# Kernel optimization log

Measured on AMD Instinct MI355X. Metric: run time of the kernel, lower is better.

Reference implementation:

```python
import jax, jax.numpy as jnp
import numpy as np

N, C_IN, T, V = 64, 64, 64, 25
C_OUT = 64
DK = DV = 16
NH = 8
DKH, DVH = DK // NH, DV // NH
KT = 9
EPS = 1e-5


def make_pe(channel, joint_num, time_len):
    # temporal positional encoding: position index = frame id, repeated per joint
    pos = np.repeat(np.arange(time_len), joint_num).astype(np.float32)[:, None]
    pe = np.zeros((time_len * joint_num, channel), np.float32)
    div = np.exp(np.arange(0, channel, 2).astype(np.float32) * -(np.log(10000.0) / channel))
    pe[:, 0::2] = np.sin(pos * div)
    pe[:, 1::2] = np.cos(pos * div)
    return jnp.asarray(pe.reshape(time_len, joint_num, channel).transpose(2, 0, 1)[None])  # (1,C,time,joint)


def setup_inputs():
    key = jax.random.key(0)
    ks = jax.random.split(key, 17)
    rn = lambda k, s, sc=0.05: jax.random.normal(k, s, jnp.float32) * sc
    return {
        'x': jax.random.normal(ks[0], (N, C_IN, T, V), jnp.float32),
        'pe': make_pe(C_IN, V, 64),
        'data_bn_g': 1.0 + rn(ks[1], (C_IN * V,)),
        'data_bn_b': rn(ks[2], (C_IN * V,)),
        'qkv_w': rn(ks[3], (3 * DK + DV, C_IN), 0.1),
        'qkv_b': rn(ks[4], (3 * DK + DV,)),
        'attn_w': rn(ks[5], (DV, DV), 0.1),
        'attn_b': rn(ks[6], (DV,)),
        'tcn_w': rn(ks[7], (C_OUT - DV, C_IN, KT, 1), 0.05),
        'tcn_b': rn(ks[8], (C_OUT - DV,)),
        'tcn_bn_g': 1.0 + rn(ks[9], (C_OUT - DV,)),
        'tcn_bn_b': rn(ks[10], (C_OUT - DV,)),
        'fc1_w': rn(ks[11], (C_OUT // 2, C_OUT), 0.1),
        'fc1_b': rn(ks[12], (C_OUT // 2,)),
        'fc2_w': rn(ks[13], (C_OUT, C_OUT // 2), 0.1),
        'fc2_b': rn(ks[14], (C_OUT,)),
        'bn_g': 1.0 + rn(ks[15], (C_OUT,)),
        'bn_b': rn(ks[16], (C_OUT,)),
    }


def _bn_eval(x, g, b, axis=1):
    # eval-mode BatchNorm with running_mean=0, running_var=1
    shape = [1] * x.ndim
    shape[axis] = -1
    scale = g / jnp.sqrt(1.0 + EPS)
    return x * scale.reshape(shape) + b.reshape(shape)


def _qkv_heads(x2d, qkv_w, qkv_b):
    # x2d: (B, C, T); 1x1 conv == channel matmul; split q/k/g/v, g is projected but unused
    qkv = jnp.einsum('oc,bct->bot', qkv_w, x2d) + qkv_b[None, :, None]
    q, k, _g, v = jnp.split(qkv, [DK, 2 * DK, 3 * DK], axis=1)
    B = x2d.shape[0]
    split = lambda z, ch: z.reshape(B, NH, ch // NH, -1)  # (B, Nh, chh, T)
    q = split(q, DK) * (DKH ** -0.5)
    return q, split(k, DK), split(v, DV)


def reference(x, pe, data_bn_g, data_bn_b, qkv_w, qkv_b, attn_w, attn_b,
              tcn_w, tcn_b, tcn_bn_g, tcn_bn_b, fc1_w, fc1_b, fc2_w, fc2_b, bn_g, bn_b):
    y = x + pe[:, :, :T]                                 # positional encoding (N,C,T,V)
    x_sum = x
    # data_bn over flattened (C*V) channels
    xb = x.transpose(0, 1, 3, 2).reshape(N, C_IN * V, T)
    xb = _bn_eval(xb, data_bn_g, data_bn_b)
    xn = xb.reshape(N, C_IN, V, T).transpose(0, 1, 3, 2)  # (N,C,T,V)
    # fold joints into batch: (N*V, C, T)
    xf = xn.transpose(0, 3, 1, 2).reshape(N * V, C_IN, T)
    yf = y.transpose(0, 3, 1, 2).reshape(N * V, C_IN, T)
    fq, fk, fv = _qkv_heads(xf, qkv_w, qkv_b)
    pq, pk, _ = _qkv_heads(yf, qkv_w, qkv_b)
    mu_q = fq.mean(-1, keepdims=True)                     # (B,H,dkh,1)
    fqc = fq - mu_q
    logits_pos = jnp.einsum('bhcs,bhct->bhst', pq, pk)    # (B,H,T,T)
    pairwise = jnp.einsum('bhcs,bhct->bhst', fqc, fk)     # (B,H,T,T)
    unary = jnp.einsum('bhcs,bhct->bhst', mu_q, fk)       # (B,H,1,T)
    weights = jnp.tanh(pairwise + logits_pos) + jnp.tanh(unary + logits_pos)
    ao = jnp.einsum('bhst,bhct->bhsc', weights, fv)       # (B,H,T,dvh)
    # (B,H,1,T,dvh) -> permute(0,1,4,2,3) -> combine heads -> (B, DV, T)
    ao = ao.transpose(0, 1, 3, 2).reshape(N * V, DV, T)
    ao = jnp.einsum('oc,bct->bot', attn_w, ao) + attn_b[None, :, None]
    ao = ao.reshape(N, V, DV, T).transpose(0, 2, 3, 1)    # (N, DV, T, V)
    # temporal conv branch (Unit2D: conv(k=9 temporal) + eval BN)
    tc = jax.lax.conv_general_dilated(x_sum, tcn_w, (1, 1), ((KT // 2, KT // 2), (0, 0)),
                                      dimension_numbers=('NCHW', 'OIHW', 'NCHW'))
    tc = tc + tcn_b[None, :, None, None]
    tc = _bn_eval(tc, tcn_bn_g, tcn_bn_b)
    result = jnp.concatenate([tc, ao], axis=1) + x_sum    # residual (down is None)
    # SE-style channel gating
    se = result.mean(axis=(2, 3))                         # (N, C_OUT)
    gate = jax.nn.sigmoid(jax.nn.relu(se @ fc1_w.T + fc1_b) @ fc2_w.T + fc2_b)
    result = result * gate[:, :, None, None] + result
    result = _bn_eval(result, bn_g, bn_b)
    return jax.nn.relu(result)
```

## Files before the change

### kernel.cpp

```cpp
#include <hip/hip_runtime.h>
#include <hip/hip_bf16.h>
#include <math.h>

#define TV_ 1600
#define SCALE_K 2.885390081777927f
#define RS2_ 0.70710678118654752f

typedef __attribute__((ext_vector_type(8))) short bf16x8;
typedef __attribute__((ext_vector_type(4))) float f32x4;
typedef __attribute__((ext_vector_type(2))) __fp16 h2f;

__device__ __forceinline__ float tanh_scaled(float y) {
    y = fminf(44.f, fmaxf(-44.f, y));
    float e = __builtin_amdgcn_exp2f(y);
    float r = __builtin_amdgcn_rcpf(e + 1.f);
    return __builtin_fmaf(e, r, -r);
}

__device__ __forceinline__ ushort f2bf(float f) {
    __hip_bfloat16 h = __float2bfloat16(f);
    return *(ushort*)&h;
}
__device__ __forceinline__ float bf2f(ushort u) {
    uint w = ((uint)u) << 16;
    return __uint_as_float(w);
}

__global__ __launch_bounds__(256) void prep_kernel(
    const float* __restrict__ tcn_w, const float* __restrict__ tg,
    const float* __restrict__ qkv_w, const float* __restrict__ qkv_b,
    const float* __restrict__ pe,
    ushort* __restrict__ wb, ushort* __restrict__ wq, float* __restrict__ qb,
    ushort* __restrict__ pet)
{
    int idx = blockIdx.x * 256 + threadIdx.x;
    if (idx < 27648) {
        int oc = idx / 576, kk = idx - oc * 576;
        int kt = kk >> 6, ci = kk & 63;
        float a = tg[oc] * rsqrtf(1.f + 1e-5f);
        wb[idx] = f2bf(tcn_w[(oc * 64 + ci) * 9 + kt] * a);
    } else if (idx < 32768) {
        int i2 = idx - 27648;
        int r = i2 >> 6, c = i2 & 63;
        int src; float sc;
        if (r < 16)      { src = r;      sc = RS2_; }
        else if (r < 32) { src = r;      sc = SCALE_K; }
        else if (r < 48) { src = r + 16; sc = 1.f; }
        else if (r < 64) { src = r - 48; sc = RS2_; }
        else             { src = r - 48; sc = SCALE_K; }
        wq[i2] = f2bf(qkv_w[src * 64 + c] * sc);
    } else if (idx < 32848) {
        int r = idx - 32768;
        int src; float sc;
        if (r < 16)      { src = r;      sc = RS2_; }
        else if (r < 32) { src = r;      sc = SCALE_K; }
        else if (r < 48) { src = r + 16; sc = 1.f; }
        else if (r < 64) { src = r - 48; sc = RS2_; }
        else             { src = r - 48; sc = SCALE_K; }
        qb[r] = qkv_b[src] * sc;
    } else if (idx < 32848 + 102400) {
        int i3 = idx - 32848;
        int ci = i3 / 1600, tv = i3 - ci * 1600;
        pet[tv * 64 + ci] = f2bf(pe[ci * 1600 + tv]);
    }
}

__global__ __launch_bounds__(256) void transpose_kernel(
    const float* __restrict__ x, ushort* __restrict__ rt, float* __restrict__ se)
{
    __shared__ ushort smt[64 * 66];
    const int tid = threadIdx.x;
    const int tv0 = blockIdx.x * 64;
    const int n = blockIdx.y;
    const int tvl = tid & 63, cig = tid >> 6;
    const int tv = tv0 + tvl;

    float psum[4] = {0.f, 0.f, 0.f, 0.f};
    #pragma unroll
    for (int k = 0; k < 16; ++k) {
        int ci = k * 4 + cig;
        float xv = x[(n * 64 + ci) * TV_ + tv];
        smt[tvl * 66 + ci] = f2bf(xv);
        if (k >= 12) psum[k - 12] += xv;
    }
    #pragma unroll
    for (int j = 0; j < 4; ++j) {
        float s = psum[j];
        #pragma unroll
        for (int off = 32; off >= 1; off >>= 1) s += __shfl_down(s, off, 64);
        if (tvl == 0) atomicAdd(&se[n * 64 + 48 + j * 4 + cig], s);
    }
    __syncthreads();

    #pragma unroll
    for (int j = 0; j < 8; ++j) {
        int chunk = tid + j * 256;
        int tvr = chunk >> 5, p = chunk & 31;
        uint val = *(const uint*)&smt[tvr * 66 + p * 2];
        *(uint*)&rt[(n * TV_ + tv0 + tvr) * 64 + p * 2] = val;
    }
}

__global__ __launch_bounds__(256, 5) void score_kernel(
    const ushort* __restrict__ rt, const ushort* __restrict__ pet,
    const float* __restrict__ dbg, const float* __restrict__ dbb,
    const ushort* __restrict__ wq, const float* __restrict__ qb,
    const float* __restrict__ attn_w, const float* __restrict__ attn_b,
    float* __restrict__ aoc, float* __restrict__ se)
{
    __shared__ float sm[5312];
    ushort* smu = (ushort*)sm;
    const int MU_ = 1056, AO = 1120;
    const int FKP = 2400, PKP = 2976, FVP = 3552, PQP = 4128, FQP = 4704;

    const int b = blockIdx.x;
    const int l = b >> 3;
    const int n = (b & 7) * 8 + l / 25;
    const int v = l % 25;
    const int tid = threadIdx.x;

    const int lane = tid & 63, wave = tid >> 6;
    const int m16 = lane & 15, q = lane >> 4;

    {
        const int part = tid & 7;
        const int ci0 = part * 8;
        const float rs = rsqrtf(1.f + 1e-5f);
        float sc8[8], sh8[8];
        #pragma unroll
        for (int i = 0; i < 8; ++i) {
            sc8[i] = dbg[(ci0 + i) * 25 + v] * rs;
            sh8[i] = dbb[(ci0 + i) * 25 + v];
        }
        #pragma unroll
        for (int j = 0; j < 2; ++j) {
            int t = (tid + j * 256) >> 3;
            uint4 xr = *(const uint4*)&rt[(n * TV_ + t * 25 + v) * 64 + ci0];
            uint4 pr = *(const uint4*)&pet[(t * 25 + v) * 64 + ci0];
            const ushort* xu = (const ushort*)&xr;
            const ushort* pu = (const ushort*)&pr;
            ushort xs[8], ys[8];
            #pragma unroll
            for (int i = 0; i < 8; ++i) {
                float xf = bf2f(xu[i]);
                xs[i] = f2bf(xf * sc8[i] + sh8[i]);
                ys[i] = f2bf(xf + bf2f(pu[i]));
            }
            *(uint4*)&smu[t * 72 + ci0] = *(uint4*)xs;
            *(uint4*)&smu[4608 + t * 72 + ci0] = *(uint4*)ys;
        }
    }
    __syncthreads();

    f32x4 acc[5];
    #pragma unroll
    for (int mt = 0; mt < 5; ++mt) acc[mt] = (f32x4){0.f, 0.f, 0.f, 0.f};
    #pragma unroll
    for (int kt = 0; kt < 2; ++kt) {
        const int koff = kt * 32 + q * 8;
        bf16x8 bx = *(const bf16x8*)&smu[(wave * 16 + m16) * 72 + koff];
        bf16x8 by = *(const bf16x8*)&smu[4608 + (wave * 16 + m16) * 72 + koff];
        #pragma unroll
        for (int mt = 0; mt < 5; ++mt) {
            bf16x8 a = *(const bf16x8*)&wq[(mt * 16 + m16) * 64 + koff];
            acc[mt] = __builtin_amdgcn_mfma_f32_16x16x32_bf16(a, (mt < 3) ? bx : by, acc[mt], 0, 0, 0);
        }
    }
    __syncthreads();

    {
        const int t = wave * 16 + m16;
        #pragma unroll
        for (int r = 0; r < 4; ++r)
            sm[(q * 4 + r) * 66 + t] = acc[0][r] + qb[q * 4 + r];
        *(h2f*)&sm[FKP + t * 9 + 2 * q] =
            __builtin_amdgcn_cvt_pkrtz(acc[1][0] + qb[16 + q * 4], acc[1][1] + qb[16 + q * 4 + 1]);
        *(h2f*)&sm[FKP + t * 9 + 2 * q + 1] =
            __builtin_amdgcn_cvt_pkrtz(acc[1][2] + qb[16 + q * 4 + 2], acc[1][3] + qb[16 + q * 4 + 3]);
        *(h2f*)&sm[FVP + t * 9 + 2 * q] =
            __builtin_amdgcn_cvt_pkrtz(acc[2][0] + qb[32 + q * 4], acc[2][1] + qb[32 + q * 4 + 1]);
        *(h2f*)&sm[FVP + t * 9 + 2 * q + 1] =
            __builtin_amdgcn_cvt_pkrtz(acc[2][2] + qb[32 + q * 4 + 2], acc[2][3] + qb[32 + q * 4 + 3]);
        *(h2f*)&sm[PQP + t * 9 + 2 * q] =
            __builtin_amdgcn_cvt_pkrtz(acc[3][0] + qb[48 + q * 4], acc[3][1] + qb[48 + q * 4 + 1]);
        *(h2f*)&sm[PQP + t * 9 + 2 * q + 1] =
            __builtin_amdgcn_cvt_pkrtz(acc[3][2] + qb[48 + q * 4 + 2], acc[3][3] + qb[48 + q * 4 + 3]);
        *(h2f*)&sm[PKP + t * 9 + 2 * q] =
            __builtin_amdgcn_cvt_pkrtz(acc[4][0] + qb[64 + q * 4], acc[4][1] + qb[64 + q * 4 + 1]);
        *(h2f*)&sm[PKP + t * 9 + 2 * q + 1] =
            __builtin_amdgcn_cvt_pkrtz(acc[4][2] + qb[64 + q * 4 + 2], acc[4][3] + qb[64 + q * 4 + 3]);
    }
    __syncthreads();

    if (tid < 64) {
        int ch = tid & 15, qq = tid >> 4;
        float s = 0.f;
        #pragma unroll
        for (int t = 0; t < 16; ++t) s += sm[ch * 66 + qq * 16 + t];
        sm[MU_ + qq * 16 + ch] = s;
    }
    __syncthreads();
    if (tid < 16) {
        float mval = (sm[MU_ + tid] + sm[MU_ + 16 + tid] + sm[MU_ + 32 + tid] + sm[MU_ + 48 + tid]) * (1.f / 64.f);
        sm[MU_ + tid] = mval;
    }
    __syncthreads();

    #pragma unroll
    for (int e = 0; e < 2; ++e) {
        int idx = tid * 2 + e;
        int s = idx >> 3, h = idx & 7;
        float a = sm[(2 * h) * 66 + s] - sm[MU_ + 2 * h];
        float c = sm[(2 * h + 1) * 66 + s] - sm[MU_ + 2 * h + 1];
        *(h2f*)&sm[FQP + s * 9 + h] = __builtin_amdgcn_cvt_pkrtz(a, c);
    }
    __syncthreads();

    const int g3 = tid & 7, m3 = tid >> 3;
    #pragma unroll 1
    for (int h = 0; h < 8; ++h) {
        const float mu0 = sm[MU_ + 2 * h], mu1 = sm[MU_ + 2 * h + 1];
        float fq0c[2], fq1c[2], pq0[2], pq1[2];
        #pragma unroll
        for (int js = 0; js < 2; ++js) {
            int s = 2 * m3 + js;
            h2f fq2 = *(const h2f*)&sm[FQP + s * 9 + h];
            h2f pq2 = *(const h2f*)&sm[PQP + s * 9 + h];
            fq0c[js] = (float)fq2.x; fq1c[js] = (float)fq2.y;
            pq0[js] = (float)pq2.x;  pq1[js] = (float)pq2.y;
        }
        float ao00 = 0.f, ao01 = 0.f, ao10 = 0.f, ao11 = 0.f;
        #pragma unroll
        for (int ch = 0; ch < 2; ++ch) {
            float fk0[4], fk1[4], pk0[4], pk1[4], fv0[4], fv1[4], un[4];
            #pragma unroll
            for (int j = 0; j < 4; ++j) {
                int t = 8 * g3 + ch * 4 + j;
                h2f fk2 = *(const h2f*)&sm[FKP + t * 9 + h];
                h2f pk2 = *(const h2f*)&sm[PKP + t * 9 + h];
                h2f fv2 = *(const h2f*)&sm[FVP + t * 9 + h];
                fk0[j] = (float)fk2.x; fk1[j] = (float)fk2.y;
                pk0[j] = (float)pk2.x; pk1[j] = (float)pk2.y;
                fv0[j] = (float)fv2.x; fv1[j] = (float)fv2.y;
                un[j] = mu0 * fk0[j] + mu1 * fk1[j];
            }
            #pragma unroll
            for (int js = 0; js < 2; ++js) {
                #pragma unroll
                for (int j = 0; j < 4; ++j) {
                    float lp = pq0[js] * pk0[j] + pq1[js] * pk1[j];
                    float a1 = fq0c[js] * fk0[j] + fq1c[js] * fk1[j] + lp;
                    float a2 = un[j] + lp;
                    float w = tanh_scaled(a1) + tanh_scaled(a2);
                    if (js == 0) { ao00 += w * fv0[j]; ao01 += w * fv1[j]; }
                    else         { ao10 += w * fv0[j]; ao11 += w * fv1[j]; }
                }
            }
        }
        #pragma unroll
        for (int off = 1; off <= 4; off <<= 1) {
            ao00 += __shfl_xor(ao00, off);
            ao01 += __shfl_xor(ao01, off);
            ao10 += __shfl_xor(ao10, off);
            ao11 += __shfl_xor(ao11, off);
        }
        if (g3 == 0) {
            sm[AO + (2 * m3) * 20 + 2 * h]         = ao00;
            sm[AO + (2 * m3) * 20 + 2 * h + 1]     = ao01;
            sm[AO + (2 * m3 + 1) * 20 + 2 * h]     = ao10;
            sm[AO + (2 * m3 + 1) * 20 + 2 * h + 1] = ao11;
        }
    }
    __syncthreads();

    const int t = tid & 63, oq = tid >> 6;
    float aorow[16];
    #pragma unroll
    for (int i = 0; i < 4; ++i)
        *(float4*)&aorow[i * 4] = *(const float4*)&sm[AO + t * 20 + i * 4];
    float* aop = aoc + (n * 25 + v) * 1024;
    #pragma unroll
    for (int j = 0; j < 4; ++j) {
        int o = oq * 4 + j;
        float acc4 = attn_b[o];
        #pragma unroll
        for (int c = 0; c < 16; ++c) acc4 += attn_w[o * 16 + c] * aorow[c];
        aop[o * 64 + t] = acc4;
        float ssum = acc4;
        #pragma unroll
        for (int off = 32; off >= 1; off >>= 1) ssum += __shfl_down(ssum, off, 64);
        if ((tid & 63) == 0) atomicAdd(&se[n * 64 + 48 + o], ssum);
    }
}

__global__ __launch_bounds__(512, 1) void tcn_mfma_kernel(
    const ushort* __restrict__ rt, const float* __restrict__ x,
    const ushort* __restrict__ wb,
    const float* __restrict__ tcn_b, const float* __restrict__ tg,
    const float* __restrict__ tb, float* __restrict__ out, float* __restrict__ se)
{
    __shared__ ushort xsl[600 * 72];
    const int b = blockIdx.x;
    const int n = b >> 2, tile = b & 3;
    const int t0 = tile * 16;
    const int tid = threadIdx.x;

    const int tvbase = (t0 - 4) * 25;
    for (int idx = tid; idx < 4800; idx += 512) {
        int r = idx >> 3, part = idx & 7;
        int tv = tvbase + r;
        uint4 val = make_uint4(0u, 0u, 0u, 0u);
        if (tv >= 0 && tv < TV_) val = *(const uint4*)&rt[(n * TV_ + tv) * 64 + part * 8];
        *(uint4*)&xsl[r * 72 + part * 8] = val;
    }
    __syncthreads();

    const int lane = tid & 63, wave = tid >> 6;
    const int m16 = lane & 15, q = lane >> 4;
    const int nt0 = wave * 3;

    f32x4 acc[3][3];
    f32x4 acc24[3];
    #pragma unroll
    for (int i = 0; i < 3; ++i)
        #pragma unroll
        for (int mt = 0; mt < 3; ++mt)
            acc[i][mt] = (f32x4){0.f, 0.f, 0.f, 0.f};
    #pragma unroll
    for (int mt = 0; mt < 3; ++mt) acc24[mt] = (f32x4){0.f, 0.f, 0.f, 0.f};

    for (int ktile = 0; ktile < 18; ++ktile) {
        const int kt = ktile >> 1;
        const int cib = (ktile & 1) * 32 + q * 8;
        bf16x8 afr[3];
        #pragma unroll
        for (int mt = 0; mt < 3; ++mt)
            afr[mt] = *(const bf16x8*)&wb[(mt * 16 + m16) * 576 + ktile * 32 + q * 8];
        #pragma unroll
        for (int i = 0; i < 3; ++i) {
            int p = (nt0 + i) * 16 + m16;
            bf16x8 bfr = *(const bf16x8*)&xsl[(p + kt * 25) * 72 + cib];
            #pragma unroll
            for (int mt = 0; mt < 3; ++mt)
                acc[i][mt] = __builtin_amdgcn_mfma_f32_16x16x32_bf16(afr[mt], bfr, acc[i][mt], 0, 0, 0);
        }
        if (wave == 0) {
            int p = 24 * 16 + m16;
            bf16x8 bfr = *(const bf16x8*)&xsl[(p + kt * 25) * 72 + cib];
            #pragma unroll
            for (int mt = 0; mt < 3; ++mt)
                acc24[mt] = __builtin_amdgcn_mfma_f32_16x16x32_bf16(afr[mt], bfr, acc24[mt], 0, 0, 0);
        }
    }

    const float rsbn = rsqrtf(1.f + 1e-5f);
    float bias3[3][4], ssum[3][4];
    #pragma unroll
    for (int mt = 0; mt < 3; ++mt)
        #pragma unroll
        for (int r = 0; r < 4; ++r) {
            int oc = mt * 16 + q * 4 + r;
            bias3[mt][r] = tcn_b[oc] * (tg[oc] * rsbn) + tb[oc];
            ssum[mt][r] = 0.f;
        }
    #pragma unroll
    for (int i = 0; i < 3; ++i) {
        int posg = tile * 400 + (nt0 + i) * 16 + m16;
        #pragma unroll
        for (int mt = 0; mt < 3; ++mt) {
            #pragma unroll
            for (int r = 0; r < 4; ++r) {
                int oc = mt * 16 + q * 4 + r;
                float val = acc[i][mt][r] + bias3[mt][r] + x[(n * 64 + oc) * TV_ + posg];
                out[(n * 64 + oc) * TV_ + posg] = val;
                ssum[mt][r] += val;
            }
        }
    }
    if (wave == 0) {
        int posg = tile * 400 + 24 * 16 + m16;
        #pragma unroll
        for (int mt = 0; mt < 3; ++mt) {
            #pragma unroll
            for (int r = 0; r < 4; ++r) {
                int oc = mt * 16 + q * 4 + r;
                float val = acc24[mt][r] + bias3[mt][r] + x[(n * 64 + oc) * TV_ + posg];
                out[(n * 64 + oc) * TV_ + posg] = val;
                ssum[mt][r] += val;
            }
        }
    }
    #pragma unroll
    for (int mt = 0; mt < 3; ++mt) {
        #pragma unroll
        for (int r = 0; r < 4; ++r) {
            float s = ssum[mt][r];
            #pragma unroll
            for (int off = 1; off <= 8; off <<= 1) s += __shfl_xor(s, off);
            if (m16 == 0) {
                int oc = mt * 16 + q * 4 + r;
                atomicAdd(&se[n * 64 + oc], s);
            }
        }
    }
}

__global__ __launch_bounds__(64) void gate_kernel(
    const float* __restrict__ se,
    const float* __restrict__ fc1w, const float* __restrict__ fc1b,
    const float* __restrict__ fc2w, const float* __restrict__ fc2b,
    float* __restrict__ gate)
{
    const int n = blockIdx.x;
    const int tid = threadIdx.x;
    __shared__ float seL[64], hid[32];
    seL[tid] = se[n * 64 + tid] * (1.f / (float)TV_);
    __syncthreads();
    if (tid < 32) {
        float a = fc1b[tid];
        #pragma unroll
        for (int c = 0; c < 64; ++c) a += fc1w[tid * 64 + c] * seL[c];
        hid[tid] = fmaxf(a, 0.f);
    }
    __syncthreads();
    float gacc = fc2b[tid];
    #pragma unroll
    for (int j = 0; j < 32; ++j) gacc += fc2w[tid * 32 + j] * hid[j];
    gate[n * 64 + tid] = 1.f / (1.f + __expf(-gacc));
}

__global__ __launch_bounds__(256) void final_kernel(
    float* __restrict__ out, const float* __restrict__ aoc,
    const float* __restrict__ x, const float* __restrict__ gate,
    const float* __restrict__ bng, const float* __restrict__ bnb)
{
    const float rs = rsqrtf(1.f + 1e-5f);
    int idx4 = blockIdx.x * 256 + threadIdx.x;
    if (idx4 >= 1638400) return;
    int nc = idx4 / 400;
    int c = nc & 63, n = nc >> 6;
    float4 val;
    if (c < 48) {
        val = ((const float4*)out)[idx4];
    } else {
        int rem = idx4 - nc * 400;
        const float* ap = aoc + n * 25600 + (c - 48) * 64;
        #pragma unroll
        for (int e = 0; e < 4; ++e) {
            int pos = rem * 4 + e;
            int t = pos / 25, v = pos - t * 25;
            ((float*)&val)[e] = ap[v * 1024 + t];
        }
        float4 xr = ((const float4*)x)[idx4];
        val.x += xr.x; val.y += xr.y; val.z += xr.z; val.w += xr.w;
    }
    float mm = (1.f + gate[nc]) * (bng[c] * rs);
    float bb = bnb[c];
    val.x = fmaxf(val.x * mm + bb, 0.f);
    val.y = fmaxf(val.y * mm + bb, 0.f);
    val.z = fmaxf(val.z * mm + bb, 0.f);
    val.w = fmaxf(val.w * mm + bb, 0.f);
    ((float4*)out)[idx4] = val;
}

extern "C" void kernel_launch(void* const* d_in, const int* in_sizes, int n_in,
                              void* d_out, int out_size, void* d_ws, size_t ws_size,
                              hipStream_t stream) {
    const float* x     = (const float*)d_in[0];
    const float* pe    = (const float*)d_in[1];
    const float* dbg   = (const float*)d_in[2];
    const float* dbb   = (const float*)d_in[3];
    const float* qkvw  = (const float*)d_in[4];
    const float* qkvb  = (const float*)d_in[5];
    const float* attnw = (const float*)d_in[6];
    const float* attnb = (const float*)d_in[7];
    const float* tcnw  = (const float*)d_in[8];
    const float* tcnb  = (const float*)d_in[9];
    const float* tcng  = (const float*)d_in[10];
    const float* tcnbb = (const float*)d_in[11];
    const float* fc1w  = (const float*)d_in[12];
    const float* fc1b  = (const float*)d_in[13];
    const float* fc2w  = (const float*)d_in[14];
    const float* fc2b  = (const float*)d_in[15];
    const float* bng   = (const float*)d_in[16];
    const float* bnb   = (const float*)d_in[17];

    float* out  = (float*)d_out;
    float* se   = (float*)d_ws;
    float* gate = se + 4096;
    float* qb   = gate + 4096;
    float* aoc  = qb + 96;
    ushort* wb  = (ushort*)(aoc + 1638400);
    ushort* wq  = wb + 27648;
    ushort* pet = wq + 5120;
    ushort* rt  = pet + 102400;

    hipMemsetAsync(se, 0, 4096 * sizeof(float), stream);
    prep_kernel<<<dim3(529), dim3(256), 0, stream>>>(tcnw, tcng, qkvw, qkvb, pe, wb, wq, qb, pet);
    transpose_kernel<<<dim3(25, 64), dim3(256), 0, stream>>>(x, rt, se);
    score_kernel<<<dim3(1600), dim3(256), 0, stream>>>(rt, pet, dbg, dbb, wq, qb, attnw, attnb, aoc, se);
    tcn_mfma_kernel<<<dim3(256), dim3(512), 0, stream>>>(rt, x, wb, tcnb, tcng, tcnbb, out, se);
    gate_kernel<<<dim3(64), dim3(64), 0, stream>>>(se, fc1w, fc1b, fc2w, fc2b, gate);
    final_kernel<<<dim3(6400), dim3(256), 0, stream>>>(out, aoc, x, gate, bng, bnb);
}
```

Baseline: 209.8 us.

## Compute TCN channel means analytically so TCN kernel writes final gated output

```diff
diff --git a/kernel.cpp b/kernel.cpp
--- a/kernel.cpp
+++ b/kernel.cpp
@@ -26,69 +26,91 @@
     return __uint_as_float(w);
 }
 
-__global__ __launch_bounds__(256) void prep_kernel(
+__global__ __launch_bounds__(256) void t1_kernel(
+    const float* __restrict__ x, const float* __restrict__ pe,
     const float* __restrict__ tcn_w, const float* __restrict__ tg,
     const float* __restrict__ qkv_w, const float* __restrict__ qkv_b,
-    const float* __restrict__ pe,
+    ushort* __restrict__ rt, float* __restrict__ Sbuf, float* __restrict__ Tt,
     ushort* __restrict__ wb, ushort* __restrict__ wq, float* __restrict__ qb,
     ushort* __restrict__ pet)
 {
-    int idx = blockIdx.x * 256 + threadIdx.x;
-    if (idx < 27648) {
-        int oc = idx / 576, kk = idx - oc * 576;
-        int kt = kk >> 6, ci = kk & 63;
-        float a = tg[oc] * rsqrtf(1.f + 1e-5f);
-        wb[idx] = f2bf(tcn_w[(oc * 64 + ci) * 9 + kt] * a);
-    } else if (idx < 32768) {
-        int i2 = idx - 27648;
-        int r = i2 >> 6, c = i2 & 63;
-        int src; float sc;
-        if (r < 16)      { src = r;      sc = RS2_; }
-        else if (r < 32) { src = r;      sc = SCALE_K; }
-        else if (r < 48) { src = r + 16; sc = 1.f; }
-        else if (r < 64) { src = r - 48; sc = RS2_; }
-        else             { src = r - 48; sc = SCALE_K; }
-        wq[i2] = f2bf(qkv_w[src * 64 + c] * sc);
-    } else if (idx < 32848) {
-        int r = idx - 32768;
-        int src; float sc;
-        if (r < 16)      { src = r;      sc = RS2_; }
-        else if (r < 32) { src = r;      sc = SCALE_K; }
-        else if (r < 48) { src = r + 16; sc = 1.f; }
-        else if (r < 64) { src = r - 48; sc = RS2_; }
-        else             { src = r - 48; sc = SCALE_K; }
-        qb[r] = qkv_b[src] * sc;
-    } else if (idx < 32848 + 102400) {
-        int i3 = idx - 32848;
-        int ci = i3 / 1600, tv = i3 - ci * 1600;
-        pet[tv * 64 + ci] = f2bf(pe[ci * 1600 + tv]);
-    }
-}
-
-__global__ __launch_bounds__(256) void transpose_kernel(
-    const float* __restrict__ x, ushort* __restrict__ rt, float* __restrict__ se)
-{
+    const int tid = threadIdx.x;
+    const int bx = blockIdx.x, by = blockIdx.y;
+
+    if (bx == 25) {
+        #pragma unroll 1
+        for (int j = 0; j < 9; ++j) {
+            int idx = by * 256 + tid + j * 16384;
+            if (idx < 27648) {
+                int oc = idx / 576, kk = idx - oc * 576;
+                int kt = kk >> 6, ci = kk & 63;
+                float a = tg[oc] * rsqrtf(1.f + 1e-5f);
+                wb[idx] = f2bf(tcn_w[(oc * 64 + ci) * 9 + kt] * a);
+            } else if (idx < 32768) {
+                int i2 = idx - 27648;
+                int r = i2 >> 6, c = i2 & 63;
+                int src; float sc;
+                if (r < 16)      { src = r;      sc = RS2_; }
+                else if (r < 32) { src = r;      sc = SCALE_K; }
+                else if (r < 48) { src = r + 16; sc = 1.f; }
+                else if (r < 64) { src = r - 48; sc = RS2_; }
+                else             { src = r - 48; sc = SCALE_K; }
+                wq[i2] = f2bf(qkv_w[src * 64 + c] * sc);
+            } else if (idx < 32848) {
+                int r = idx - 32768;
+                int src; float sc;
+                if (r < 16)      { src = r;      sc = RS2_; }
+                else if (r < 32) { src = r;      sc = SCALE_K; }
+                else if (r < 48) { src = r + 16; sc = 1.f; }
+                else if (r < 64) { src = r - 48; sc = RS2_; }
+                else             { src = r - 48; sc = SCALE_K; }
+                qb[r] = qkv_b[src] * sc;
+            } else if (idx < 135248) {
+                int i3 = idx - 32848;
+                int ci = i3 / 1600, tv = i3 - ci * 1600;
+                pet[tv * 64 + ci] = f2bf(pe[ci * 1600 + tv]);
+            }
+        }
+        return;
+    }
+    if (bx == 26) {
+        const int n = by;
+        #pragma unroll
+        for (int it = 0; it < 2; ++it) {
+            int item = tid + it * 256;
+            int ci = item >> 3, slot = item & 7;
+            int t = (slot < 4) ? slot : (56 + slot);
+            const float* xp = x + (n * 64 + ci) * TV_ + t * 25;
+            float s = 0.f;
+            #pragma unroll
+            for (int v = 0; v < 25; ++v) s += xp[v];
+            Tt[(n * 64 + ci) * 8 + slot] = s;
+        }
+        return;
+    }
+
     __shared__ ushort smt[64 * 66];
-    const int tid = threadIdx.x;
-    const int tv0 = blockIdx.x * 64;
-    const int n = blockIdx.y;
+    const int tv0 = bx * 64;
+    const int n = by;
     const int tvl = tid & 63, cig = tid >> 6;
     const int tv = tv0 + tvl;
 
-    float psum[4] = {0.f, 0.f, 0.f, 0.f};
+    float psum[16];
+    #pragma unroll
+    for (int k = 0; k < 16; ++k) psum[k] = 0.f;
     #pragma unroll
     for (int k = 0; k < 16; ++k) {
         int ci = k * 4 + cig;
         float xv = x[(n * 64 + ci) * TV_ + tv];
         smt[tvl * 66 + ci] = f2bf(xv);
-        if (k >= 12) psum[k - 12] += xv;
-    }
-    #pragma unroll
-    for (int j = 0; j < 4; ++j) {
-        float s = psum[j];
+        psum[k] += xv;
+    }
+    #pragma unroll
+    for (int k = 0; k < 16; ++k) {
+        float s = psum[k];
         #pragma unroll
         for (int off = 32; off >= 1; off >>= 1) s += __shfl_down(s, off, 64);
-        if (tvl == 0) atomicAdd(&se[n * 64 + 48 + j * 4 + cig], s);
+        if (tvl == 0) atomicAdd(&Sbuf[n * 64 + k * 4 + cig], s);
     }
     __syncthreads();
 
@@ -113,191 +135,261 @@
     const int MU_ = 1056, AO = 1120;
     const int FKP = 2400, PKP = 2976, FVP = 3552, PQP = 4128, FQP = 4704;
 
-    const int b = blockIdx.x;
-    const int l = b >> 3;
-    const int n = (b & 7) * 8 + l / 25;
-    const int v = l % 25;
     const int tid = threadIdx.x;
-
     const int lane = tid & 63, wave = tid >> 6;
     const int m16 = lane & 15, q = lane >> 4;
 
-    {
-        const int part = tid & 7;
-        const int ci0 = part * 8;
-        const float rs = rsqrtf(1.f + 1e-5f);
-        float sc8[8], sh8[8];
-        #pragma unroll
-        for (int i = 0; i < 8; ++i) {
-            sc8[i] = dbg[(ci0 + i) * 25 + v] * rs;
-            sh8[i] = dbb[(ci0 + i) * 25 + v];
-        }
-        #pragma unroll
-        for (int j = 0; j < 2; ++j) {
-            int t = (tid + j * 256) >> 3;
-            uint4 xr = *(const uint4*)&rt[(n * TV_ + t * 25 + v) * 64 + ci0];
-            uint4 pr = *(const uint4*)&pet[(t * 25 + v) * 64 + ci0];
-            const ushort* xu = (const ushort*)&xr;
-            const ushort* pu = (const ushort*)&pr;
-            ushort xs[8], ys[8];
+    #pragma unroll 1
+    for (int it = 0; it < 2; ++it) {
+        if (it) __syncthreads();
+        const int l = blockIdx.x * 2 + it;
+        const int n = l / 25, v = l % 25;
+
+        {
+            const int part = tid & 7;
+            const int ci0 = part * 8;
+            const float rs = rsqrtf(1.f + 1e-5f);
+            float sc8[8], sh8[8];
             #pragma unroll
             for (int i = 0; i < 8; ++i) {
-                float xf = bf2f(xu[i]);
-                xs[i] = f2bf(xf * sc8[i] + sh8[i]);
-                ys[i] = f2bf(xf + bf2f(pu[i]));
-            }
-            *(uint4*)&smu[t * 72 + ci0] = *(uint4*)xs;
-            *(uint4*)&smu[4608 + t * 72 + ci0] = *(uint4*)ys;
-        }
-    }
-    __syncthreads();
-
-    f32x4 acc[5];
-    #pragma unroll
-    for (int mt = 0; mt < 5; ++mt) acc[mt] = (f32x4){0.f, 0.f, 0.f, 0.f};
-    #pragma unroll
-    for (int kt = 0; kt < 2; ++kt) {
-        const int koff = kt * 32 + q * 8;
-        bf16x8 bx = *(const bf16x8*)&smu[(wave * 16 + m16) * 72 + koff];
-        bf16x8 by = *(const bf16x8*)&smu[4608 + (wave * 16 + m16) * 72 + koff];
-        #pragma unroll
-        for (int mt = 0; mt < 5; ++mt) {
-            bf16x8 a = *(const bf16x8*)&wq[(mt * 16 + m16) * 64 + koff];
-            acc[mt] = __builtin_amdgcn_mfma_f32_16x16x32_bf16(a, (mt < 3) ? bx : by, acc[mt], 0, 0, 0);
-        }
-    }
-    __syncthreads();
-
-    {
-        const int t = wave * 16 + m16;
-        #pragma unroll
-        for (int r = 0; r < 4; ++r)
-            sm[(q * 4 + r) * 66 + t] = acc[0][r] + qb[q * 4 + r];
-        *(h2f*)&sm[FKP + t * 9 + 2 * q] =
-            __builtin_amdgcn_cvt_pkrtz(acc[1][0] + qb[16 + q * 4], acc[1][1] + qb[16 + q * 4 + 1]);
-        *(h2f*)&sm[FKP + t * 9 + 2 * q + 1] =
-            __builtin_amdgcn_cvt_pkrtz(acc[1][2] + qb[16 + q * 4 + 2], acc[1][3] + qb[16 + q * 4 + 3]);
-        *(h2f*)&sm[FVP + t * 9 + 2 * q] =
-            __builtin_amdgcn_cvt_pkrtz(acc[2][0] + qb[32 + q * 4], acc[2][1] + qb[32 + q * 4 + 1]);
-        *(h2f*)&sm[FVP + t * 9 + 2 * q + 1] =
-            __builtin_amdgcn_cvt_pkrtz(acc[2][2] + qb[32 + q * 4 + 2], acc[2][3] + qb[32 + q * 4 + 3]);
-        *(h2f*)&sm[PQP + t * 9 + 2 * q] =
-            __builtin_amdgcn_cvt_pkrtz(acc[3][0] + qb[48 + q * 4], acc[3][1] + qb[48 + q * 4 + 1]);
-        *(h2f*)&sm[PQP + t * 9 + 2 * q + 1] =
-            __builtin_amdgcn_cvt_pkrtz(acc[3][2] + qb[48 + q * 4 + 2], acc[3][3] + qb[48 + q * 4 + 3]);
-        *(h2f*)&sm[PKP + t * 9 + 2 * q] =
-            __builtin_amdgcn_cvt_pkrtz(acc[4][0] + qb[64 + q * 4], acc[4][1] + qb[64 + q * 4 + 1]);
-        *(h2f*)&sm[PKP + t * 9 + 2 * q + 1] =
-            __builtin_amdgcn_cvt_pkrtz(acc[4][2] + qb[64 + q * 4 + 2], acc[4][3] + qb[64 + q * 4 + 3]);
-    }
-    __syncthreads();
-
-    if (tid < 64) {
-        int ch = tid & 15, qq = tid >> 4;
-        float s = 0.f;
-        #pragma unroll
-        for (int t = 0; t < 16; ++t) s += sm[ch * 66 + qq * 16 + t];
-        sm[MU_ + qq * 16 + ch] = s;
-    }
-    __syncthreads();
-    if (tid < 16) {
-        float mval = (sm[MU_ + tid] + sm[MU_ + 16 + tid] + sm[MU_ + 32 + tid] + sm[MU_ + 48 + tid]) * (1.f / 64.f);
-        sm[MU_ + tid] = mval;
-    }
-    __syncthreads();
-
-    #pragma unroll
-    for (int e = 0; e < 2; ++e) {
-        int idx = tid * 2 + e;
-        int s = idx >> 3, h = idx & 7;
-        float a = sm[(2 * h) * 66 + s] - sm[MU_ + 2 * h];
-        float c = sm[(2 * h + 1) * 66 + s] - sm[MU_ + 2 * h + 1];
-        *(h2f*)&sm[FQP + s * 9 + h] = __builtin_amdgcn_cvt_pkrtz(a, c);
-    }
-    __syncthreads();
-
-    const int g3 = tid & 7, m3 = tid >> 3;
-    #pragma unroll 1
-    for (int h = 0; h < 8; ++h) {
-        const float mu0 = sm[MU_ + 2 * h], mu1 = sm[MU_ + 2 * h + 1];
-        float fq0c[2], fq1c[2], pq0[2], pq1[2];
-        #pragma unroll
-        for (int js = 0; js < 2; ++js) {
-            int s = 2 * m3 + js;
-            h2f fq2 = *(const h2f*)&sm[FQP + s * 9 + h];
-            h2f pq2 = *(const h2f*)&sm[PQP + s * 9 + h];
-            fq0c[js] = (float)fq2.x; fq1c[js] = (float)fq2.y;
-            pq0[js] = (float)pq2.x;  pq1[js] = (float)pq2.y;
-        }
-        float ao00 = 0.f, ao01 = 0.f, ao10 = 0.f, ao11 = 0.f;
-        #pragma unroll
-        for (int ch = 0; ch < 2; ++ch) {
-            float fk0[4], fk1[4], pk0[4], pk1[4], fv0[4], fv1[4], un[4];
-            #pragma unroll
-            for (int j = 0; j < 4; ++j) {
-                int t = 8 * g3 + ch * 4 + j;
-                h2f fk2 = *(const h2f*)&sm[FKP + t * 9 + h];
-                h2f pk2 = *(const h2f*)&sm[PKP + t * 9 + h];
-                h2f fv2 = *(const h2f*)&sm[FVP + t * 9 + h];
-                fk0[j] = (float)fk2.x; fk1[j] = (float)fk2.y;
-                pk0[j] = (float)pk2.x; pk1[j] = (float)pk2.y;
-                fv0[j] = (float)fv2.x; fv1[j] = (float)fv2.y;
-                un[j] = mu0 * fk0[j] + mu1 * fk1[j];
-            }
+                sc8[i] = dbg[(ci0 + i) * 25 + v] * rs;
+                sh8[i] = dbb[(ci0 + i) * 25 + v];
+            }
+            #pragma unroll
+            for (int j = 0; j < 2; ++j) {
+                int t = (tid + j * 256) >> 3;
+                uint4 xr = *(const uint4*)&rt[(n * TV_ + t * 25 + v) * 64 + ci0];
+                uint4 pr = *(const uint4*)&pet[(t * 25 + v) * 64 + ci0];
+                const ushort* xu = (const ushort*)&xr;
+                const ushort* pu = (const ushort*)&pr;
+                ushort xs[8], ys[8];
+                #pragma unroll
+                for (int i = 0; i < 8; ++i) {
+                    float xf = bf2f(xu[i]);
+                    xs[i] = f2bf(xf * sc8[i] + sh8[i]);
+                    ys[i] = f2bf(xf + bf2f(pu[i]));
+                }
+                *(uint4*)&smu[t * 72 + ci0] = *(uint4*)xs;
+                *(uint4*)&smu[4608 + t * 72 + ci0] = *(uint4*)ys;
+            }
+        }
+        __syncthreads();
+
+        f32x4 acc[5];
+        #pragma unroll
+        for (int mt = 0; mt < 5; ++mt) acc[mt] = (f32x4){0.f, 0.f, 0.f, 0.f};
+        #pragma unroll
+        for (int kt = 0; kt < 2; ++kt) {
+            const int koff = kt * 32 + q * 8;
+            bf16x8 bx = *(const bf16x8*)&smu[(wave * 16 + m16) * 72 + koff];
+            bf16x8 by = *(const bf16x8*)&smu[4608 + (wave * 16 + m16) * 72 + koff];
+            #pragma unroll
+            for (int mt = 0; mt < 5; ++mt) {
+                bf16x8 a = *(const bf16x8*)&wq[(mt * 16 + m16) * 64 + koff];
+                acc[mt] = __builtin_amdgcn_mfma_f32_16x16x32_bf16(a, (mt < 3) ? bx : by, acc[mt], 0, 0, 0);
+            }
+        }
+        __syncthreads();
+
+        {
+            const int t = wave * 16 + m16;
+            #pragma unroll
+            for (int r = 0; r < 4; ++r)
+                sm[(q * 4 + r) * 66 + t] = acc[0][r] + qb[q * 4 + r];
+            *(h2f*)&sm[FKP + t * 9 + 2 * q] =
+                __builtin_amdgcn_cvt_pkrtz(acc[1][0] + qb[16 + q * 4], acc[1][1] + qb[16 + q * 4 + 1]);
+            *(h2f*)&sm[FKP + t * 9 + 2 * q + 1] =
+                __builtin_amdgcn_cvt_pkrtz(acc[1][2] + qb[16 + q * 4 + 2], acc[1][3] + qb[16 + q * 4 + 3]);
+            *(h2f*)&sm[FVP + t * 9 + 2 * q] =
+                __builtin_amdgcn_cvt_pkrtz(acc[2][0] + qb[32 + q * 4], acc[2][1] + qb[32 + q * 4 + 1]);
+            *(h2f*)&sm[FVP + t * 9 + 2 * q + 1] =
+                __builtin_amdgcn_cvt_pkrtz(acc[2][2] + qb[32 + q * 4 + 2], acc[2][3] + qb[32 + q * 4 + 3]);
+            *(h2f*)&sm[PQP + t * 9 + 2 * q] =
+                __builtin_amdgcn_cvt_pkrtz(acc[3][0] + qb[48 + q * 4], acc[3][1] + qb[48 + q * 4 + 1]);
+            *(h2f*)&sm[PQP + t * 9 + 2 * q + 1] =
+                __builtin_amdgcn_cvt_pkrtz(acc[3][2] + qb[48 + q * 4 + 2], acc[3][3] + qb[48 + q * 4 + 3]);
+            *(h2f*)&sm[PKP + t * 9 + 2 * q] =
+                __builtin_amdgcn_cvt_pkrtz(acc[4][0] + qb[64 + q * 4], acc[4][1] + qb[64 + q * 4 + 1]);
+            *(h2f*)&sm[PKP + t * 9 + 2 * q + 1] =
+                __builtin_amdgcn_cvt_pkrtz(acc[4][2] + qb[64 + q * 4 + 2], acc[4][3] + qb[64 + q * 4 + 3]);
+        }
+        __syncthreads();
+
+        if (tid < 64) {
+            int ch = tid & 15, qq = tid >> 4;
+            float s = 0.f;
+            #pragma unroll
+            for (int t = 0; t < 16; ++t) s += sm[ch * 66 + qq * 16 + t];
+            sm[MU_ + qq * 16 + ch] = s;
+        }
+        __syncthreads();
+        if (tid < 16) {
+            float mval = (sm[MU_ + tid] + sm[MU_ + 16 + tid] + sm[MU_ + 32 + tid] + sm[MU_ + 48 + tid]) * (1.f / 64.f);
+            sm[MU_ + tid] = mval;
+        }
+        __syncthreads();
+
+        #pragma unroll
+        for (int e = 0; e < 2; ++e) {
+            int idx = tid * 2 + e;
+            int s = idx >> 3, h = idx & 7;
+            float a = sm[(2 * h) * 66 + s] - sm[MU_ + 2 * h];
+            float c = sm[(2 * h + 1) * 66 + s] - sm[MU_ + 2 * h + 1];
+            *(h2f*)&sm[FQP + s * 9 + h] = __builtin_amdgcn_cvt_pkrtz(a, c);
+        }
+        __syncthreads();
+
+        const int g3 = tid & 7, m3 = tid >> 3;
+        #pragma unroll 1
+        for (int h = 0; h < 8; ++h) {
+            const float mu0 = sm[MU_ + 2 * h], mu1 = sm[MU_ + 2 * h + 1];
+            float fq0c[2], fq1c[2], pq0[2], pq1[2];
             #pragma unroll
             for (int js = 0; js < 2; ++js) {
+                int s = 2 * m3 + js;
+                h2f fq2 = *(const h2f*)&sm[FQP + s * 9 + h];
+                h2f pq2 = *(const h2f*)&sm[PQP + s * 9 + h];
+                fq0c[js] = (float)fq2.x; fq1c[js] = (float)fq2.y;
+                pq0[js] = (float)pq2.x;  pq1[js] = (float)pq2.y;
+            }
+            float ao00 = 0.f, ao01 = 0.f, ao10 = 0.f, ao11 = 0.f;
+            #pragma unroll
+            for (int ch = 0; ch < 2; ++ch) {
+                float fk0[4], fk1[4], pk0[4], pk1[4], fv0[4], fv1[4], un[4];
                 #pragma unroll
                 for (int j = 0; j < 4; ++j) {
-                    float lp = pq0[js] * pk0[j] + pq1[js] * pk1[j];
-                    float a1 = fq0c[js] * fk0[j] + fq1c[js] * fk1[j] + lp;
-                    float a2 = un[j] + lp;
-                    float w = tanh_scaled(a1) + tanh_scaled(a2);
-                    if (js == 0) { ao00 += w * fv0[j]; ao01 += w * fv1[j]; }
-                    else         { ao10 += w * fv0[j]; ao11 += w * fv1[j]; }
+                    int t = 8 * g3 + ch * 4 + j;
+                    h2f fk2 = *(const h2f*)&sm[FKP + t * 9 + h];
+                    h2f pk2 = *(const h2f*)&sm[PKP + t * 9 + h];
+                    h2f fv2 = *(const h2f*)&sm[FVP + t * 9 + h];
+                    fk0[j] = (float)fk2.x; fk1[j] = (float)fk2.y;
+                    pk0[j] = (float)pk2.x; pk1[j] = (float)pk2.y;
+                    fv0[j] = (float)fv2.x; fv1[j] = (float)fv2.y;
+                    un[j] = mu0 * fk0[j] + mu1 * fk1[j];
                 }
-            }
-        }
-        #pragma unroll
-        for (int off = 1; off <= 4; off <<= 1) {
-            ao00 += __shfl_xor(ao00, off);
-            ao01 += __shfl_xor(ao01, off);
-            ao10 += __shfl_xor(ao10, off);
-            ao11 += __shfl_xor(ao11, off);
-        }
-        if (g3 == 0) {
-            sm[AO + (2 * m3) * 20 + 2 * h]         = ao00;
-            sm[AO + (2 * m3) * 20 + 2 * h + 1]     = ao01;
-            sm[AO + (2 * m3 + 1) * 20 + 2 * h]     = ao10;
-            sm[AO + (2 * m3 + 1) * 20 + 2 * h + 1] = ao11;
-        }
+                #pragma unroll
+                for (int js = 0; js < 2; ++js) {
+                    #pragma unroll
+                    for (int j = 0; j < 4; ++j) {
+                        float lp = pq0[js] * pk0[j] + pq1[js] * pk1[j];
+                        float a1 = fq0c[js] * fk0[j] + fq1c[js] * fk1[j] + lp;
+                        float a2 = un[j] + lp;
+                        float w = tanh_scaled(a1) + tanh_scaled(a2);
+                        if (js == 0) { ao00 += w * fv0[j]; ao01 += w * fv1[j]; }
+                        else         { ao10 += w * fv0[j]; ao11 += w * fv1[j]; }
+                    }
+                }
+            }
+            #pragma unroll
+            for (int off = 1; off <= 4; off <<= 1) {
+                ao00 += __shfl_xor(ao00, off);
+                ao01 += __shfl_xor(ao01, off);
+                ao10 += __shfl_xor(ao10, off);
+                ao11 += __shfl_xor(ao11, off);
+            }
+            if (g3 == 0) {
+                sm[AO + (2 * m3) * 20 + 2 * h]         = ao00;
+                sm[AO + (2 * m3) * 20 + 2 * h + 1]     = ao01;
+                sm[AO + (2 * m3 + 1) * 20 + 2 * h]     = ao10;
+                sm[AO + (2 * m3 + 1) * 20 + 2 * h + 1] = ao11;
+            }
+        }
+        __syncthreads();
+
+        const int t = tid & 63, oq = tid >> 6;
+        float aorow[16];
+        #pragma unroll
+        for (int i = 0; i < 4; ++i)
+            *(float4*)&aorow[i * 4] = *(const float4*)&sm[AO + t * 20 + i * 4];
+        float* aop = aoc + (n * 25 + v) * 1024;
+        #pragma unroll
+        for (int j = 0; j < 4; ++j) {
+            int o = oq * 4 + j;
+            float acc4 = attn_b[o];
+            #pragma unroll
+            for (int c = 0; c < 16; ++c) acc4 += attn_w[o * 16 + c] * aorow[c];
+            aop[o * 64 + t] = acc4;
+            float ssum = acc4;
+            #pragma unroll
+            for (int off = 32; off >= 1; off >>= 1) ssum += __shfl_down(ssum, off, 64);
+            if ((tid & 63) == 0) atomicAdd(&se[n * 64 + 48 + o], ssum);
+        }
+    }
+}
+
+__global__ __launch_bounds__(64) void gate_kernel(
+    const float* __restrict__ se, const float* __restrict__ Sbuf,
+    const float* __restrict__ Tt, const ushort* __restrict__ wb,
+    const float* __restrict__ tcn_b, const float* __restrict__ tg,
+    const float* __restrict__ tb,
+    const float* __restrict__ fc1w, const float* __restrict__ fc1b,
+    const float* __restrict__ fc2w, const float* __restrict__ fc2b,
+    float* __restrict__ gate)
+{
+    const int n = blockIdx.x;
+    const int tid = threadIdx.x;
+    __shared__ float U[64][9], seL[64], hid[32];
+    const float rs = rsqrtf(1.f + 1e-5f);
+
+    {
+        int ci = tid;
+        float S = Sbuf[n * 64 + ci];
+        float T[8];
+        #pragma unroll
+        for (int j = 0; j < 8; ++j) T[j] = Tt[(n * 64 + ci) * 8 + j];
+        U[ci][0] = S - (T[4] + T[5] + T[6] + T[7]);
+        U[ci][1] = S - (T[5] + T[6] + T[7]);
+        U[ci][2] = S - (T[6] + T[7]);
+        U[ci][3] = S - T[7];
+        U[ci][4] = S;
+        U[ci][5] = S - T[0];
+        U[ci][6] = S - (T[0] + T[1]);
+        U[ci][7] = S - (T[0] + T[1] + T[2]);
+        U[ci][8] = S - (T[0] + T[1] + T[2] + T[3]);
     }
     __syncthreads();
 
-    const int t = tid & 63, oq = tid >> 6;
-    float aorow[16];
-    #pragma unroll
-    for (int i = 0; i < 4; ++i)
-        *(float4*)&aorow[i * 4] = *(const float4*)&sm[AO + t * 20 + i * 4];
-    float* aop = aoc + (n * 25 + v) * 1024;
-    #pragma unroll
-    for (int j = 0; j < 4; ++j) {
-        int o = oq * 4 + j;
-        float acc4 = attn_b[o];
-        #pragma unroll
-        for (int c = 0; c < 16; ++c) acc4 += attn_w[o * 16 + c] * aorow[c];
-        aop[o * 64 + t] = acc4;
-        float ssum = acc4;
-        #pragma unroll
-        for (int off = 32; off >= 1; off >>= 1) ssum += __shfl_down(ssum, off, 64);
-        if ((tid & 63) == 0) atomicAdd(&se[n * 64 + 48 + o], ssum);
-    }
+    if (tid < 48) {
+        int oc = tid;
+        float cs = 0.f;
+        #pragma unroll 1
+        for (int kt = 0; kt < 9; ++kt) {
+            #pragma unroll
+            for (int cb = 0; cb < 8; ++cb) {
+                bf16x8 w8 = *(const bf16x8*)&wb[oc * 576 + kt * 64 + cb * 8];
+                #pragma unroll
+                for (int i = 0; i < 8; ++i)
+                    cs += bf2f((ushort)w8[i]) * U[cb * 8 + i][kt];
+            }
+        }
+        float a = tg[oc] * rs;
+        float cb_ = tcn_b[oc] * a + tb[oc];
+        seL[oc] = (a * cs + 1600.f * cb_ + Sbuf[n * 64 + oc]) * (1.f / 1600.f);
+    } else {
+        int c = tid + 0;
+        seL[c] = (se[n * 64 + c] + Sbuf[n * 64 + c]) * (1.f / 1600.f);
+    }
+    __syncthreads();
+    if (tid < 32) {
+        float a = fc1b[tid];
+        #pragma unroll
+        for (int c = 0; c < 64; ++c) a += fc1w[tid * 64 + c] * seL[c];
+        hid[tid] = fmaxf(a, 0.f);
+    }
+    __syncthreads();
+    float g = fc2b[tid];
+    #pragma unroll
+    for (int j = 0; j < 32; ++j) g += fc2w[tid * 32 + j] * hid[j];
+    gate[n * 64 + tid] = 1.f / (1.f + __expf(-g));
 }
 
 __global__ __launch_bounds__(512, 1) void tcn_mfma_kernel(
     const ushort* __restrict__ rt, const float* __restrict__ x,
     const ushort* __restrict__ wb,
     const float* __restrict__ tcn_b, const float* __restrict__ tg,
-    const float* __restrict__ tb, float* __restrict__ out, float* __restrict__ se)
+    const float* __restrict__ tb, const float* __restrict__ gate,
+    const float* __restrict__ bng, const float* __restrict__ bnb,
+    float* __restrict__ out)
 {
     __shared__ ushort xsl[600 * 72];
     const int b = blockIdx.x;
@@ -354,14 +446,16 @@
     }
 
     const float rsbn = rsqrtf(1.f + 1e-5f);
-    float bias3[3][4], ssum[3][4];
+    float cb3[3][4], m3_[3][4], bb3[3][4];
     #pragma unroll
     for (int mt = 0; mt < 3; ++mt)
         #pragma unroll
         for (int r = 0; r < 4; ++r) {
             int oc = mt * 16 + q * 4 + r;
-            bias3[mt][r] = tcn_b[oc] * (tg[oc] * rsbn) + tb[oc];
-            ssum[mt][r] = 0.f;
+            float a = tg[oc] * rsbn;
+            cb3[mt][r] = tcn_b[oc] * a + tb[oc];
+            m3_[mt][r] = (1.f + gate[n * 64 + oc]) * (bng[oc] * rsbn);
+            bb3[mt][r] = bnb[oc];
         }
     #pragma unroll
     for (int i = 0; i < 3; ++i) {
@@ -371,9 +465,8 @@
             #pragma unroll
             for (int r = 0; r < 4; ++r) {
                 int oc = mt * 16 + q * 4 + r;
-                float val = acc[i][mt][r] + bias3[mt][r] + x[(n * 64 + oc) * TV_ + posg];
-                out[(n * 64 + oc) * TV_ + posg] = val;
-                ssum[mt][r] += val;
+                float val = acc[i][mt][r] + cb3[mt][r] + x[(n * 64 + oc) * TV_ + posg];
+                out[(n * 64 + oc) * TV_ + posg] = fmaxf(val * m3_[mt][r] + bb3[mt][r], 0.f);
             }
         }
     }
@@ -384,49 +477,11 @@
             #pragma unroll
             for (int r = 0; r < 4; ++r) {
                 int oc = mt * 16 + q * 4 + r;
-                float val = acc24[mt][r] + bias3[mt][r] + x[(n * 64 + oc) * TV_ + posg];
-                out[(n * 64 + oc) * TV_ + posg] = val;
-                ssum[mt][r] += val;
-            }
-        }
-    }
-    #pragma unroll
-    for (int mt = 0; mt < 3; ++mt) {
-        #pragma unroll
-        for (int r = 0; r < 4; ++r) {
-            float s = ssum[mt][r];
-            #pragma unroll
-            for (int off = 1; off <= 8; off <<= 1) s += __shfl_xor(s, off);
-            if (m16 == 0) {
-                int oc = mt * 16 + q * 4 + r;
-                atomicAdd(&se[n * 64 + oc], s);
-            }
-        }
-    }
-}
-
-__global__ __launch_bounds__(64) void gate_kernel(
-    const float* __restrict__ se,
-    const float* __restrict__ fc1w, const float* __restrict__ fc1b,
-    const float* __restrict__ fc2w, const float* __restrict__ fc2b,
-    float* __restrict__ gate)
-{
-    const int n = blockIdx.x;
-    const int tid = threadIdx.x;
-    __shared__ float seL[64], hid[32];
-    seL[tid] = se[n * 64 + tid] * (1.f / (float)TV_);
-    __syncthreads();
-    if (tid < 32) {
-        float a = fc1b[tid];
-        #pragma unroll
-        for (int c = 0; c < 64; ++c) a += fc1w[tid * 64 + c] * seL[c];
-        hid[tid] = fmaxf(a, 0.f);
-    }
-    __syncthreads();
-    float gacc = fc2b[tid];
-    #pragma unroll
-    for (int j = 0; j < 32; ++j) gacc += fc2w[tid * 32 + j] * hid[j];
-    gate[n * 64 + tid] = 1.f / (1.f + __expf(-gacc));
+                float val = acc24[mt][r] + cb3[mt][r] + x[(n * 64 + oc) * TV_ + posg];
+                out[(n * 64 + oc) * TV_ + posg] = fmaxf(val * m3_[mt][r] + bb3[mt][r], 0.f);
+            }
+        }
+    }
 }
 
 __global__ __launch_bounds__(256) void final_kernel(
@@ -435,32 +490,28 @@
     const float* __restrict__ bng, const float* __restrict__ bnb)
 {
     const float rs = rsqrtf(1.f + 1e-5f);
-    int idx4 = blockIdx.x * 256 + threadIdx.x;
-    if (idx4 >= 1638400) return;
-    int nc = idx4 / 400;
-    int c = nc & 63, n = nc >> 6;
+    int idx = blockIdx.x * 256 + threadIdx.x;
+    int n = idx / 6400;
+    int rem = idx - n * 6400;
+    int o = rem / 400, r4 = rem - o * 400;
+
     float4 val;
-    if (c < 48) {
-        val = ((const float4*)out)[idx4];
-    } else {
-        int rem = idx4 - nc * 400;
-        const float* ap = aoc + n * 25600 + (c - 48) * 64;
-        #pragma unroll
-        for (int e = 0; e < 4; ++e) {
-            int pos = rem * 4 + e;
-            int t = pos / 25, v = pos - t * 25;
-            ((float*)&val)[e] = ap[v * 1024 + t];
-        }
-        float4 xr = ((const float4*)x)[idx4];
-        val.x += xr.x; val.y += xr.y; val.z += xr.z; val.w += xr.w;
-    }
-    float mm = (1.f + gate[nc]) * (bng[c] * rs);
-    float bb = bnb[c];
-    val.x = fmaxf(val.x * mm + bb, 0.f);
-    val.y = fmaxf(val.y * mm + bb, 0.f);
-    val.z = fmaxf(val.z * mm + bb, 0.f);
-    val.w = fmaxf(val.w * mm + bb, 0.f);
-    ((float4*)out)[idx4] = val;
+    const float* ap = aoc + (n * 25) * 1024 + o * 64;
+    #pragma unroll
+    for (int e = 0; e < 4; ++e) {
+        int pos = r4 * 4 + e;
+        int t = pos / 25, v = pos - t * 25;
+        ((float*)&val)[e] = ap[v * 1024 + t];
+    }
+    int g4 = (n * 64 + 48 + o) * 400 + r4;
+    float4 xr = ((const float4*)x)[g4];
+    float mm = (1.f + gate[n * 64 + 48 + o]) * (bng[48 + o] * rs);
+    float bb = bnb[48 + o];
+    val.x = fmaxf((val.x + xr.x) * mm + bb, 0.f);
+    val.y = fmaxf((val.y + xr.y) * mm + bb, 0.f);
+    val.z = fmaxf((val.z + xr.z) * mm + bb, 0.f);
+    val.w = fmaxf((val.w + xr.w) * mm + bb, 0.f);
+    ((float4*)out)[g4] = val;
 }
 
 extern "C" void kernel_launch(void* const* d_in, const int* in_sizes, int n_in,
@@ -487,7 +538,9 @@
 
     float* out  = (float*)d_out;
     float* se   = (float*)d_ws;
-    float* gate = se + 4096;
+    float* Sbuf = se + 4096;
+    float* Tt   = Sbuf + 4096;
+    float* gate = Tt + 32768;
     float* qb   = gate + 4096;
     float* aoc  = qb + 96;
     ushort* wb  = (ushort*)(aoc + 1638400);
@@ -495,11 +548,13 @@
     ushort* pet = wq + 5120;
     ushort* rt  = pet + 102400;
 
-    hipMemsetAsync(se, 0, 4096 * sizeof(float), stream);
-    prep_kernel<<<dim3(529), dim3(256), 0, stream>>>(tcnw, tcng, qkvw, qkvb, pe, wb, wq, qb, pet);
-    transpose_kernel<<<dim3(25, 64), dim3(256), 0, stream>>>(x, rt, se);
-    score_kernel<<<dim3(1600), dim3(256), 0, stream>>>(rt, pet, dbg, dbb, wq, qb, attnw, attnb, aoc, se);
-    tcn_mfma_kernel<<<dim3(256), dim3(512), 0, stream>>>(rt, x, wb, tcnb, tcng, tcnbb, out, se);
-    gate_kernel<<<dim3(64), dim3(64), 0, stream>>>(se, fc1w, fc1b, fc2w, fc2b, gate);
-    final_kernel<<<dim3(6400), dim3(256), 0, stream>>>(out, aoc, x, gate, bng, bnb);
-}
+    hipMemsetAsync(se, 0, (4096 + 4096) * sizeof(float), stream);
+    t1_kernel<<<dim3(27, 64), dim3(256), 0, stream>>>(
+        x, pe, tcnw, tcng, qkvw, qkvb, rt, Sbuf, Tt, wb, wq, qb, pet);
+    score_kernel<<<dim3(800), dim3(256), 0, stream>>>(rt, pet, dbg, dbb, wq, qb, attnw, attnb, aoc, se);
+    gate_kernel<<<dim3(64), dim3(64), 0, stream>>>(
+        se, Sbuf, Tt, wb, tcnb, tcng, tcnbb, fc1w, fc1b, fc2w, fc2b, gate);
+    tcn_mfma_kernel<<<dim3(256), dim3(512), 0, stream>>>(
+        rt, x, wb, tcnb, tcng, tcnbb, gate, bng, bnb, out);
+    final_kernel<<<dim3(1600), dim3(256), 0, stream>>>(out, aoc, x, gate, bng, bnb);
+}
```

Result: slower. 278.3 us (+32.7%).
